# Kernel optimization log

Measured on AMD Instinct MI355X. Metric: run time of the kernel, lower is better.

Reference implementation:

```python
import jax, jax.numpy as jnp
import numpy as np

IN_F = 4096
OUT_F = 4096
SPARSITY = 0.9
NNZ = round((1.0 - SPARSITY) * IN_F * OUT_F)  # 1677722
BATCH = 4096


def setup_inputs() -> dict:
    key = jax.random.key(0)
    k1, k2, k3, k4 = jax.random.split(key, 4)
    x = jax.random.normal(k1, (BATCH, IN_F), dtype=jnp.float32)
    # Kaiming-ish scale for sparse fan-in
    weights = jax.random.normal(k2, (NNZ,), dtype=jnp.float32) * 0.02
    row = jax.random.randint(k3, (NNZ,), 0, OUT_F, dtype=jnp.int32)
    col = jax.random.randint(k4, (NNZ,), 0, IN_F, dtype=jnp.int32)
    indices = jnp.stack([row, col], axis=0)  # (2, nnz) like the torch buffer
    active_mask = jnp.ones((NNZ,), dtype=bool)
    return {
        "x": x,
        "weights": weights,
        "indices": indices,
        "active_mask": active_mask,
        "out_features": OUT_F,
        "in_features": IN_F,
    }


def reference(x, weights, indices, active_mask, out_features, in_features):
    # Torch forward: select active edges, build COO (out,in), coalesce
    # (sums duplicate indices), then y = (W @ x^T)^T.
    # Equivalent math: zero inactive weights, scatter-add into dense W,
    # then a dense matmul. Duplicates are summed by .add, matching coalesce.
    w = jnp.where(active_mask, weights, jnp.zeros((), dtype=weights.dtype))
    W = jnp.zeros((out_features, in_features), dtype=x.dtype)
    W = W.at[indices[0], indices[1]].add(w)  # (out, in)
    return x @ W.T  # (B, out)
```

## Files before the change

kernel.cpp:

```cpp
#include <hip/hip_runtime.h>
#include <cstdint>
#include <cstddef>

#define IN_F  4096
#define OUT_F 4096
#define BATCH 4096

typedef __bf16 bf16_t;
typedef __bf16 bf16x8 __attribute__((ext_vector_type(8)));
typedef float  f32x4  __attribute__((ext_vector_type(4)));

__device__ __forceinline__ unsigned short f32_to_bf16_rne(float f) {
  union { float f; unsigned int u; } v;
  v.f = f;
  unsigned int u = v.u;
  return (unsigned short)((u + 0x7FFFu + ((u >> 16) & 1u)) >> 16);
}

__device__ __forceinline__ uint4 cvt8(float4 a, float4 b) {
  uint4 o;
  o.x = (unsigned)f32_to_bf16_rne(a.x) | ((unsigned)f32_to_bf16_rne(a.y) << 16);
  o.y = (unsigned)f32_to_bf16_rne(a.z) | ((unsigned)f32_to_bf16_rne(a.w) << 16);
  o.z = (unsigned)f32_to_bf16_rne(b.x) | ((unsigned)f32_to_bf16_rne(b.y) << 16);
  o.w = (unsigned)f32_to_bf16_rne(b.z) | ((unsigned)f32_to_bf16_rne(b.w) << 16);
  return o;
}

#define WUNITS ((OUT_F * IN_F) / 8)
#define XUNITS ((BATCH * IN_F) / 8)

__global__ __launch_bounds__(256) void init_zero_cvtx(
    float4* __restrict__ Wf32v, const float4* __restrict__ xin,
    uint4* __restrict__ xbf) {
  const float4 z = {0.f, 0.f, 0.f, 0.f};
  for (int u = blockIdx.x * 256 + threadIdx.x; u < WUNITS + XUNITS;
       u += gridDim.x * 256) {
    if (u < WUNITS) {
      Wf32v[2 * u]     = z;
      Wf32v[2 * u + 1] = z;
    } else {
      const int i = u - WUNITS;
      xbf[i] = cvt8(xin[2 * i], xin[2 * i + 1]);
    }
  }
}

__global__ __launch_bounds__(256) void scatter_kernel(
    const float* __restrict__ w, const int* __restrict__ rows,
    const int* __restrict__ cols, const int* __restrict__ mask,
    float* __restrict__ W, int nnz) {
  int i = blockIdx.x * 256 + threadIdx.x;
  if (i < nnz) {
    if (mask[i] != 0) {
      atomicAdd(&W[(size_t)rows[i] * IN_F + cols[i]], w[i]);
    }
  }
}

__global__ __launch_bounds__(256) void cvt_f32_bf16(
    const float4* __restrict__ in, uint4* __restrict__ out, int n8) {
  int i = blockIdx.x * 256 + threadIdx.x;
  if (i >= n8) return;
  out[i] = cvt8(in[2 * i], in[2 * i + 1]);
}

#define A0_B 0
#define B0_B 32768
#define A1_B 65536
#define B1_B 98304
#define HALF 16384

#define STAGE(Xg, kpos, ldsbase) do {                                          \
  __builtin_amdgcn_global_load_lds(                                            \
    (const __attribute__((address_space(1))) void*)((Xg) + (size_t)srow * 4096 + (kpos) + schunk), \
    (__attribute__((address_space(3))) void*)(lds + (ldsbase) + tid * 16), 16, 0, 0); \
  __builtin_amdgcn_global_load_lds(                                            \
    (const __attribute__((address_space(1))) void*)((Xg) + (size_t)(srow + 128) * 4096 + (kpos) + schunk), \
    (__attribute__((address_space(3))) void*)(lds + (ldsbase) + 8192 + tid * 16), 16, 0, 0); \
} while (0)

#define LDA4(base, mh) do {                                                    \
  a0 = *(const bf16x8*)(lds + (base) + offA[mh][0]);                           \
  a1 = *(const bf16x8*)(lds + (base) + offA[mh][1]);                           \
  a2 = *(const bf16x8*)(lds + (base) + offA[mh][2]);                           \
  a3 = *(const bf16x8*)(lds + (base) + offA[mh][3]);                           \
} while (0)

#define LDB4(base) do {                                                        \
  b0 = *(const bf16x8*)(lds + (base) + offB[0]);                               \
  b1 = *(const bf16x8*)(lds + (base) + offB[1]);                               \
  b2 = *(const bf16x8*)(lds + (base) + offB[2]);                               \
  b3 = *(const bf16x8*)(lds + (base) + offB[3]);                               \
} while (0)

#define MFMA16(mh) do {                                                        \
  acc[(mh)*4+0][0] = __builtin_amdgcn_mfma_f32_16x16x32_bf16(a0, b0, acc[(mh)*4+0][0], 0, 0, 0); \
  acc[(mh)*4+0][1] = __builtin_amdgcn_mfma_f32_16x16x32_bf16(a0, b1, acc[(mh)*4+0][1], 0, 0, 0); \
  acc[(mh)*4+0][2] = __builtin_amdgcn_mfma_f32_16x16x32_bf16(a0, b2, acc[(mh)*4+0][2], 0, 0, 0); \
  acc[(mh)*4+0][3] = __builtin_amdgcn_mfma_f32_16x16x32_bf16(a0, b3, acc[(mh)*4+0][3], 0, 0, 0); \
  acc[(mh)*4+1][0] = __builtin_amdgcn_mfma_f32_16x16x32_bf16(a1, b0, acc[(mh)*4+1][0], 0, 0, 0); \
  acc[(mh)*4+1][1] = __builtin_amdgcn_mfma_f32_16x16x32_bf16(a1, b1, acc[(mh)*4+1][1], 0, 0, 0); \
  acc[(mh)*4+1][2] = __builtin_amdgcn_mfma_f32_16x16x32_bf16(a1, b2, acc[(mh)*4+1][2], 0, 0, 0); \
  acc[(mh)*4+1][3] = __builtin_amdgcn_mfma_f32_16x16x32_bf16(a1, b3, acc[(mh)*4+1][3], 0, 0, 0); \
  acc[(mh)*4+2][0] = __builtin_amdgcn_mfma_f32_16x16x32_bf16(a2, b0, acc[(mh)*4+2][0], 0, 0, 0); \
  acc[(mh)*4+2][1] = __builtin_amdgcn_mfma_f32_16x16x32_bf16(a2, b1, acc[(mh)*4+2][1], 0, 0, 0); \
  acc[(mh)*4+2][2] = __builtin_amdgcn_mfma_f32_16x16x32_bf16(a2, b2, acc[(mh)*4+2][2], 0, 0, 0); \
  acc[(mh)*4+2][3] = __builtin_amdgcn_mfma_f32_16x16x32_bf16(a2, b3, acc[(mh)*4+2][3], 0, 0, 0); \
  acc[(mh)*4+3][0] = __builtin_amdgcn_mfma_f32_16x16x32_bf16(a3, b0, acc[(mh)*4+3][0], 0, 0, 0); \
  acc[(mh)*4+3][1] = __builtin_amdgcn_mfma_f32_16x16x32_bf16(a3, b1, acc[(mh)*4+3][1], 0, 0, 0); \
  acc[(mh)*4+3][2] = __builtin_amdgcn_mfma_f32_16x16x32_bf16(a3, b2, acc[(mh)*4+3][2], 0, 0, 0); \
  acc[(mh)*4+3][3] = __builtin_amdgcn_mfma_f32_16x16x32_bf16(a3, b3, acc[(mh)*4+3][3], 0, 0, 0); \
} while (0)

#define BAR()   __builtin_amdgcn_s_barrier()
#define LGKM0() do { asm volatile("s_waitcnt lgkmcnt(0)" ::: "memory");        \
                     __builtin_amdgcn_sched_barrier(0); } while (0)
#define VM(n)   asm volatile("s_waitcnt vmcnt(" #n ")" ::: "memory")
#define PRIO1() __builtin_amdgcn_s_setprio(1)
#define PRIO0() __builtin_amdgcn_s_setprio(0)

__global__ __launch_bounds__(512, 2) void gemm_bt_8ph(
    const bf16_t* __restrict__ A, const bf16_t* __restrict__ Bm,
    float* __restrict__ C) {
  __shared__ __align__(16) char lds[131072];

  const int tid  = threadIdx.x;
  const int lane = tid & 63;
  const int wave = tid >> 6;
  const int wm   = wave >> 2;
  const int wn   = wave & 3;

  const int sbid = (blockIdx.x & 7) * 32 + (blockIdx.x >> 3);
  const int bm   = sbid >> 4;
  const int bn   = sbid & 15;

  const int frow = lane & 15;
  const int c16  = (lane >> 4) * 16;

  int offA[2][4], offB[4];
#pragma unroll
  for (int mh = 0; mh < 2; ++mh)
#pragma unroll
    for (int mi = 0; mi < 4; ++mi) {
      int r = wm * 128 + mh * 64 + mi * 16 + frow;
      offA[mh][mi] = r * 64 + (c16 ^ (((r >> 1) & 3) << 4));
    }
#pragma unroll
  for (int ni = 0; ni < 4; ++ni) {
    int r = wn * 64 + ni * 16 + frow;
    offB[ni] = r * 64 + (c16 ^ (((r >> 1) & 3) << 4));
  }

  const int srow   = tid >> 2;
  const int schunk = ((tid & 3) ^ ((srow >> 1) & 3)) * 8;
  const bf16_t* Ag = A  + (size_t)bm * 256 * 4096;
  const bf16_t* Bg = Bm + (size_t)bn * 256 * 4096;

  f32x4 acc[8][4] = {};
  bf16x8 a0, a1, a2, a3, b0, b1, b2, b3;

  STAGE(Ag, 0,  A0_B);
  STAGE(Bg, 0,  B0_B);
  STAGE(Ag, 32, A0_B + HALF);
  STAGE(Bg, 32, B0_B + HALF);
  STAGE(Bg, 64, B1_B);
  STAGE(Ag, 64, A1_B);
  STAGE(Bg, 96, B1_B + HALF);
  VM(6);
  BAR();

  int kb = 0;
#pragma unroll 1
  for (int i = 0; i < 31; ++i, kb += 128) {
    LDA4(A0_B, 0); LDB4(B0_B);
    STAGE(Ag, kb + 96, A1_B + HALF);
    BAR(); LGKM0(); PRIO1(); MFMA16(0); PRIO0(); BAR();
    LDA4(A0_B, 1);
    STAGE(Bg, kb + 128, B0_B);
    BAR(); LGKM0(); PRIO1(); MFMA16(1); PRIO0(); VM(10); BAR();
    LDA4(A0_B + HALF, 0); LDB4(B0_B + HALF);
    STAGE(Ag, kb + 128, A0_B);
    BAR(); LGKM0(); PRIO1(); MFMA16(0); PRIO0(); BAR();
    LDA4(A0_B + HALF, 1);
    STAGE(Bg, kb + 160, B0_B + HALF);
    BAR(); LGKM0(); PRIO1(); MFMA16(1); PRIO0(); VM(10); BAR();
    LDA4(A1_B, 0); LDB4(B1_B);
    STAGE(Ag, kb + 160, A0_B + HALF);
    BAR(); LGKM0(); PRIO1(); MFMA16(0); PRIO0(); BAR();
    LDA4(A1_B, 1);
    STAGE(Bg, kb + 192, B1_B);
    BAR(); LGKM0(); PRIO1(); MFMA16(1); PRIO0(); VM(10); BAR();
    LDA4(A1_B + HALF, 0); LDB4(B1_B + HALF);
    STAGE(Ag, kb + 192, A1_B);
    BAR(); LGKM0(); PRIO1(); MFMA16(0); PRIO0(); BAR();
    LDA4(A1_B + HALF, 1);
    STAGE(Bg, kb + 224, B1_B + HALF);
    BAR(); LGKM0(); PRIO1(); MFMA16(1); PRIO0(); VM(10); BAR();
  }

  LDA4(A0_B, 0); LDB4(B0_B);
  STAGE(Ag, 4064, A1_B + HALF);
  BAR(); LGKM0(); PRIO1(); MFMA16(0); PRIO0(); BAR();
  LDA4(A0_B, 1);
  BAR(); LGKM0(); PRIO1(); MFMA16(1); PRIO0(); VM(6); BAR();
  LDA4(A0_B + HALF, 0); LDB4(B0_B + HALF);
  BAR(); LGKM0(); PRIO1(); MFMA16(0); PRIO0(); BAR();
  LDA4(A0_B + HALF, 1);
  BAR(); LGKM0(); PRIO1(); MFMA16(1); PRIO0(); VM(2); BAR();
  LDA4(A1_B, 0); LDB4(B1_B);
  BAR(); LGKM0(); PRIO1(); MFMA16(0); PRIO0(); BAR();
  LDA4(A1_B, 1);
  BAR(); LGKM0(); PRIO1(); MFMA16(1); PRIO0(); VM(0); BAR();
  LDA4(A1_B + HALF, 0); LDB4(B1_B + HALF);
  BAR(); LGKM0(); PRIO1(); MFMA16(0); PRIO0(); BAR();
  LDA4(A1_B + HALF, 1);
  LGKM0(); PRIO1(); MFMA16(1); PRIO0();

#pragma unroll
  for (int mh = 0; mh < 2; ++mh)
#pragma unroll
    for (int mi = 0; mi < 4; ++mi)
#pragma unroll
      for (int ni = 0; ni < 4; ++ni) {
        const int row = bm * 256 + wm * 128 + mh * 64 + mi * 16 + (lane >> 4) * 4;
        const int col = bn * 256 + wn * 64 + ni * 16 + frow;
#pragma unroll
        for (int jj = 0; jj < 4; ++jj)
          C[(size_t)(row + jj) * 4096 + col] = acc[mh * 4 + mi][ni][jj];
      }
}

extern "C" void kernel_launch(void* const* d_in, const int* in_sizes, int n_in,
                              void* d_out, int out_size, void* d_ws, size_t ws_size,
                              hipStream_t stream) {
  const float* x     = (const float*)d_in[0];
  const float* wvals = (const float*)d_in[1];
  const int*   idx   = (const int*)d_in[2];
  const int*   mk    = (const int*)d_in[3];
  const int    nnz   = in_sizes[1];

  float*  Wf32 = (float*)d_out;
  bf16_t* Wbf  = (bf16_t*)d_ws;
  bf16_t* xbf  = (bf16_t*)((char*)d_ws + (size_t)OUT_F * IN_F * sizeof(bf16_t));

  const size_t needed = (size_t)OUT_F * IN_F * 2 + (size_t)BATCH * IN_F * 2;
  if (ws_size < needed) return;

  init_zero_cvtx<<<2048, 256, 0, stream>>>(
      (float4*)Wf32, (const float4*)x, (uint4*)xbf);

  scatter_kernel<<<(nnz + 255) / 256, 256, 0, stream>>>(
      wvals, idx, idx + nnz, mk, Wf32, nnz);

  const int w8 = (OUT_F * IN_F) / 8;
  cvt_f32_bf16<<<(w8 + 255) / 256, 256, 0, stream>>>(
      (const float4*)Wf32, (uint4*)Wbf, w8);

  gemm_bt_8ph<<<256, 512, 0, stream>>>(xbf, Wbf, (float*)d_out);
}
```

Measured before the change: 227.7 us.

## Scatter directly into bf16 weights via packed atomics and merge GEMM phases

The scatter now converts each weight to bf16 and accumulates it directly into a bf16 dense W with global_atomic_pk_add_bf16. This removes the fp32 W zeroing (64 MB of writes) and the separate fp32-to-bf16 conversion pass. Duplicate indices are now summed in bf16, which can change rounding compared with summing in fp32. The GEMM main loop also moves from 8 phases to 4 by loading all A/B fragments at once and issuing 32 MFMAs per phase, with fewer barriers but more registers held live.

```diff
diff --git a/kernel.cpp b/kernel.cpp
--- a/kernel.cpp
+++ b/kernel.cpp
@@ -26,42 +26,37 @@
   return o;
 }
 
-#define WUNITS ((OUT_F * IN_F) / 8)
+#define WU16 ((OUT_F * IN_F) / 8)
 #define XUNITS ((BATCH * IN_F) / 8)
 
 __global__ __launch_bounds__(256) void init_zero_cvtx(
-    float4* __restrict__ Wf32v, const float4* __restrict__ xin,
+    uint4* __restrict__ Wbfv, const float4* __restrict__ xin,
     uint4* __restrict__ xbf) {
-  const float4 z = {0.f, 0.f, 0.f, 0.f};
-  for (int u = blockIdx.x * 256 + threadIdx.x; u < WUNITS + XUNITS;
+  const uint4 z = {0u, 0u, 0u, 0u};
+  for (int u = blockIdx.x * 256 + threadIdx.x; u < WU16 + XUNITS;
        u += gridDim.x * 256) {
-    if (u < WUNITS) {
-      Wf32v[2 * u]     = z;
-      Wf32v[2 * u + 1] = z;
+    if (u < WU16) {
+      Wbfv[u] = z;
     } else {
-      const int i = u - WUNITS;
+      const int i = u - WU16;
       xbf[i] = cvt8(xin[2 * i], xin[2 * i + 1]);
     }
   }
 }
 
-__global__ __launch_bounds__(256) void scatter_kernel(
+__global__ __launch_bounds__(256) void scatter_bf16(
     const float* __restrict__ w, const int* __restrict__ rows,
     const int* __restrict__ cols, const int* __restrict__ mask,
-    float* __restrict__ W, int nnz) {
+    unsigned* __restrict__ Wpk, int nnz) {
   int i = blockIdx.x * 256 + threadIdx.x;
-  if (i < nnz) {
-    if (mask[i] != 0) {
-      atomicAdd(&W[(size_t)rows[i] * IN_F + cols[i]], w[i]);
-    }
-  }
-}
-
-__global__ __launch_bounds__(256) void cvt_f32_bf16(
-    const float4* __restrict__ in, uint4* __restrict__ out, int n8) {
-  int i = blockIdx.x * 256 + threadIdx.x;
-  if (i >= n8) return;
-  out[i] = cvt8(in[2 * i], in[2 * i + 1]);
+  if (i >= nnz) return;
+  if (mask[i] == 0) return;
+  const unsigned h = f32_to_bf16_rne(w[i]);
+  const size_t e = (size_t)rows[i] * IN_F + cols[i];
+  const unsigned data = (e & 1) ? (h << 16) : h;
+  unsigned* p = Wpk + (e >> 1);
+  asm volatile("global_atomic_pk_add_bf16 %0, %1, off"
+               :: "v"(p), "v"(data) : "memory");
 }
 
 #define A0_B 0
@@ -79,38 +74,41 @@
     (__attribute__((address_space(3))) void*)(lds + (ldsbase) + 8192 + tid * 16), 16, 0, 0); \
 } while (0)
 
-#define LDA4(base, mh) do {                                                    \
-  a0 = *(const bf16x8*)(lds + (base) + offA[mh][0]);                           \
-  a1 = *(const bf16x8*)(lds + (base) + offA[mh][1]);                           \
-  a2 = *(const bf16x8*)(lds + (base) + offA[mh][2]);                           \
-  a3 = *(const bf16x8*)(lds + (base) + offA[mh][3]);                           \
+#define LDALL(ab, bb) do {                                                     \
+  a0 = *(const bf16x8*)(lds + (ab) + offA[0][0]);                              \
+  a1 = *(const bf16x8*)(lds + (ab) + offA[0][1]);                              \
+  a2 = *(const bf16x8*)(lds + (ab) + offA[0][2]);                              \
+  a3 = *(const bf16x8*)(lds + (ab) + offA[0][3]);                              \
+  a4 = *(const bf16x8*)(lds + (ab) + offA[1][0]);                              \
+  a5 = *(const bf16x8*)(lds + (ab) + offA[1][1]);                              \
+  a6 = *(const bf16x8*)(lds + (ab) + offA[1][2]);                              \
+  a7 = *(const bf16x8*)(lds + (ab) + offA[1][3]);                              \
+  b0 = *(const bf16x8*)(lds + (bb) + offB[0]);                                 \
+  b1 = *(const bf16x8*)(lds + (bb) + offB[1]);                                 \
+  b2 = *(const bf16x8*)(lds + (bb) + offB[2]);                                 \
+  b3 = *(const bf16x8*)(lds + (bb) + offB[3]);                                 \
 } while (0)
 
-#define LDB4(base) do {                                                        \
-  b0 = *(const bf16x8*)(lds + (base) + offB[0]);                               \
-  b1 = *(const bf16x8*)(lds + (base) + offB[1]);                               \
-  b2 = *(const bf16x8*)(lds + (base) + offB[2]);                               \
-  b3 = *(const bf16x8*)(lds + (base) + offB[3]);                               \
+#define MQ(mh, A0_, A1_, A2_, A3_) do {                                        \
+  acc[(mh)*4+0][0] = __builtin_amdgcn_mfma_f32_16x16x32_bf16(A0_, b0, acc[(mh)*4+0][0], 0, 0, 0); \
+  acc[(mh)*4+0][1] = __builtin_amdgcn_mfma_f32_16x16x32_bf16(A0_, b1, acc[(mh)*4+0][1], 0, 0, 0); \
+  acc[(mh)*4+0][2] = __builtin_amdgcn_mfma_f32_16x16x32_bf16(A0_, b2, acc[(mh)*4+0][2], 0, 0, 0); \
+  acc[(mh)*4+0][3] = __builtin_amdgcn_mfma_f32_16x16x32_bf16(A0_, b3, acc[(mh)*4+0][3], 0, 0, 0); \
+  acc[(mh)*4+1][0] = __builtin_amdgcn_mfma_f32_16x16x32_bf16(A1_, b0, acc[(mh)*4+1][0], 0, 0, 0); \
+  acc[(mh)*4+1][1] = __builtin_amdgcn_mfma_f32_16x16x32_bf16(A1_, b1, acc[(mh)*4+1][1], 0, 0, 0); \
+  acc[(mh)*4+1][2] = __builtin_amdgcn_mfma_f32_16x16x32_bf16(A1_, b2, acc[(mh)*4+1][2], 0, 0, 0); \
+  acc[(mh)*4+1][3] = __builtin_amdgcn_mfma_f32_16x16x32_bf16(A1_, b3, acc[(mh)*4+1][3], 0, 0, 0); \
+  acc[(mh)*4+2][0] = __builtin_amdgcn_mfma_f32_16x16x32_bf16(A2_, b0, acc[(mh)*4+2][0], 0, 0, 0); \
+  acc[(mh)*4+2][1] = __builtin_amdgcn_mfma_f32_16x16x32_bf16(A2_, b1, acc[(mh)*4+2][1], 0, 0, 0); \
+  acc[(mh)*4+2][2] = __builtin_amdgcn_mfma_f32_16x16x32_bf16(A2_, b2, acc[(mh)*4+2][2], 0, 0, 0); \
+  acc[(mh)*4+2][3] = __builtin_amdgcn_mfma_f32_16x16x32_bf16(A2_, b3, acc[(mh)*4+2][3], 0, 0, 0); \
+  acc[(mh)*4+3][0] = __builtin_amdgcn_mfma_f32_16x16x32_bf16(A3_, b0, acc[(mh)*4+3][0], 0, 0, 0); \
+  acc[(mh)*4+3][1] = __builtin_amdgcn_mfma_f32_16x16x32_bf16(A3_, b1, acc[(mh)*4+3][1], 0, 0, 0); \
+  acc[(mh)*4+3][2] = __builtin_amdgcn_mfma_f32_16x16x32_bf16(A3_, b2, acc[(mh)*4+3][2], 0, 0, 0); \
+  acc[(mh)*4+3][3] = __builtin_amdgcn_mfma_f32_16x16x32_bf16(A3_, b3, acc[(mh)*4+3][3], 0, 0, 0); \
 } while (0)
 
-#define MFMA16(mh) do {                                                        \
-  acc[(mh)*4+0][0] = __builtin_amdgcn_mfma_f32_16x16x32_bf16(a0, b0, acc[(mh)*4+0][0], 0, 0, 0); \
-  acc[(mh)*4+0][1] = __builtin_amdgcn_mfma_f32_16x16x32_bf16(a0, b1, acc[(mh)*4+0][1], 0, 0, 0); \
-  acc[(mh)*4+0][2] = __builtin_amdgcn_mfma_f32_16x16x32_bf16(a0, b2, acc[(mh)*4+0][2], 0, 0, 0); \
-  acc[(mh)*4+0][3] = __builtin_amdgcn_mfma_f32_16x16x32_bf16(a0, b3, acc[(mh)*4+0][3], 0, 0, 0); \
-  acc[(mh)*4+1][0] = __builtin_amdgcn_mfma_f32_16x16x32_bf16(a1, b0, acc[(mh)*4+1][0], 0, 0, 0); \
-  acc[(mh)*4+1][1] = __builtin_amdgcn_mfma_f32_16x16x32_bf16(a1, b1, acc[(mh)*4+1][1], 0, 0, 0); \
-  acc[(mh)*4+1][2] = __builtin_amdgcn_mfma_f32_16x16x32_bf16(a1, b2, acc[(mh)*4+1][2], 0, 0, 0); \
-  acc[(mh)*4+1][3] = __builtin_amdgcn_mfma_f32_16x16x32_bf16(a1, b3, acc[(mh)*4+1][3], 0, 0, 0); \
-  acc[(mh)*4+2][0] = __builtin_amdgcn_mfma_f32_16x16x32_bf16(a2, b0, acc[(mh)*4+2][0], 0, 0, 0); \
-  acc[(mh)*4+2][1] = __builtin_amdgcn_mfma_f32_16x16x32_bf16(a2, b1, acc[(mh)*4+2][1], 0, 0, 0); \
-  acc[(mh)*4+2][2] = __builtin_amdgcn_mfma_f32_16x16x32_bf16(a2, b2, acc[(mh)*4+2][2], 0, 0, 0); \
-  acc[(mh)*4+2][3] = __builtin_amdgcn_mfma_f32_16x16x32_bf16(a2, b3, acc[(mh)*4+2][3], 0, 0, 0); \
-  acc[(mh)*4+3][0] = __builtin_amdgcn_mfma_f32_16x16x32_bf16(a3, b0, acc[(mh)*4+3][0], 0, 0, 0); \
-  acc[(mh)*4+3][1] = __builtin_amdgcn_mfma_f32_16x16x32_bf16(a3, b1, acc[(mh)*4+3][1], 0, 0, 0); \
-  acc[(mh)*4+3][2] = __builtin_amdgcn_mfma_f32_16x16x32_bf16(a3, b2, acc[(mh)*4+3][2], 0, 0, 0); \
-  acc[(mh)*4+3][3] = __builtin_amdgcn_mfma_f32_16x16x32_bf16(a3, b3, acc[(mh)*4+3][3], 0, 0, 0); \
-} while (0)
+#define MFMA32() do { MQ(0, a0, a1, a2, a3); MQ(1, a4, a5, a6, a7); } while (0)
 
 #define BAR()   __builtin_amdgcn_s_barrier()
 #define LGKM0() do { asm volatile("s_waitcnt lgkmcnt(0)" ::: "memory");        \
@@ -119,7 +117,7 @@
 #define PRIO1() __builtin_amdgcn_s_setprio(1)
 #define PRIO0() __builtin_amdgcn_s_setprio(0)
 
-__global__ __launch_bounds__(512, 2) void gemm_bt_8ph(
+__global__ __launch_bounds__(512, 2) void gemm_bt_4ph(
     const bf16_t* __restrict__ A, const bf16_t* __restrict__ Bm,
     float* __restrict__ C) {
   __shared__ __align__(16) char lds[131072];
@@ -157,64 +155,48 @@
   const bf16_t* Bg = Bm + (size_t)bn * 256 * 4096;
 
   f32x4 acc[8][4] = {};
-  bf16x8 a0, a1, a2, a3, b0, b1, b2, b3;
+  bf16x8 a0, a1, a2, a3, a4, a5, a6, a7, b0, b1, b2, b3;
 
   STAGE(Ag, 0,  A0_B);
   STAGE(Bg, 0,  B0_B);
   STAGE(Ag, 32, A0_B + HALF);
   STAGE(Bg, 32, B0_B + HALF);
+  STAGE(Ag, 64, A1_B);
   STAGE(Bg, 64, B1_B);
-  STAGE(Ag, 64, A1_B);
-  STAGE(Bg, 96, B1_B + HALF);
-  VM(6);
+  VM(8);
   BAR();
 
   int kb = 0;
 #pragma unroll 1
   for (int i = 0; i < 31; ++i, kb += 128) {
-    LDA4(A0_B, 0); LDB4(B0_B);
+    LDALL(A0_B, B0_B);
     STAGE(Ag, kb + 96, A1_B + HALF);
-    BAR(); LGKM0(); PRIO1(); MFMA16(0); PRIO0(); BAR();
-    LDA4(A0_B, 1);
+    STAGE(Bg, kb + 96, B1_B + HALF);
+    BAR(); LGKM0(); PRIO1(); MFMA32(); PRIO0(); VM(8); BAR();
+    LDALL(A0_B + HALF, B0_B + HALF);
+    STAGE(Ag, kb + 128, A0_B);
     STAGE(Bg, kb + 128, B0_B);
-    BAR(); LGKM0(); PRIO1(); MFMA16(1); PRIO0(); VM(10); BAR();
-    LDA4(A0_B + HALF, 0); LDB4(B0_B + HALF);
-    STAGE(Ag, kb + 128, A0_B);
-    BAR(); LGKM0(); PRIO1(); MFMA16(0); PRIO0(); BAR();
-    LDA4(A0_B + HALF, 1);
+    BAR(); LGKM0(); PRIO1(); MFMA32(); PRIO0(); VM(8); BAR();
+    LDALL(A1_B, B1_B);
+    STAGE(Ag, kb + 160, A0_B + HALF);
     STAGE(Bg, kb + 160, B0_B + HALF);
-    BAR(); LGKM0(); PRIO1(); MFMA16(1); PRIO0(); VM(10); BAR();
-    LDA4(A1_B, 0); LDB4(B1_B);
-    STAGE(Ag, kb + 160, A0_B + HALF);
-    BAR(); LGKM0(); PRIO1(); MFMA16(0); PRIO0(); BAR();
-    LDA4(A1_B, 1);
+    BAR(); LGKM0(); PRIO1(); MFMA32(); PRIO0(); VM(8); BAR();
+    LDALL(A1_B + HALF, B1_B + HALF);
+    STAGE(Ag, kb + 192, A1_B);
     STAGE(Bg, kb + 192, B1_B);
-    BAR(); LGKM0(); PRIO1(); MFMA16(1); PRIO0(); VM(10); BAR();
-    LDA4(A1_B + HALF, 0); LDB4(B1_B + HALF);
-    STAGE(Ag, kb + 192, A1_B);
-    BAR(); LGKM0(); PRIO1(); MFMA16(0); PRIO0(); BAR();
-    LDA4(A1_B + HALF, 1);
-    STAGE(Bg, kb + 224, B1_B + HALF);
-    BAR(); LGKM0(); PRIO1(); MFMA16(1); PRIO0(); VM(10); BAR();
+    BAR(); LGKM0(); PRIO1(); MFMA32(); PRIO0(); VM(8); BAR();
   }
 
-  LDA4(A0_B, 0); LDB4(B0_B);
+  LDALL(A0_B, B0_B);
   STAGE(Ag, 4064, A1_B + HALF);
-  BAR(); LGKM0(); PRIO1(); MFMA16(0); PRIO0(); BAR();
-  LDA4(A0_B, 1);
-  BAR(); LGKM0(); PRIO1(); MFMA16(1); PRIO0(); VM(6); BAR();
-  LDA4(A0_B + HALF, 0); LDB4(B0_B + HALF);
-  BAR(); LGKM0(); PRIO1(); MFMA16(0); PRIO0(); BAR();
-  LDA4(A0_B + HALF, 1);
-  BAR(); LGKM0(); PRIO1(); MFMA16(1); PRIO0(); VM(2); BAR();
-  LDA4(A1_B, 0); LDB4(B1_B);
-  BAR(); LGKM0(); PRIO1(); MFMA16(0); PRIO0(); BAR();
-  LDA4(A1_B, 1);
-  BAR(); LGKM0(); PRIO1(); MFMA16(1); PRIO0(); VM(0); BAR();
-  LDA4(A1_B + HALF, 0); LDB4(B1_B + HALF);
-  BAR(); LGKM0(); PRIO1(); MFMA16(0); PRIO0(); BAR();
-  LDA4(A1_B + HALF, 1);
-  LGKM0(); PRIO1(); MFMA16(1); PRIO0();
+  STAGE(Bg, 4064, B1_B + HALF);
+  BAR(); LGKM0(); PRIO1(); MFMA32(); PRIO0(); VM(8); BAR();
+  LDALL(A0_B + HALF, B0_B + HALF);
+  BAR(); LGKM0(); PRIO1(); MFMA32(); PRIO0(); VM(4); BAR();
+  LDALL(A1_B, B1_B);
+  BAR(); LGKM0(); PRIO1(); MFMA32(); PRIO0(); VM(0); BAR();
+  LDALL(A1_B + HALF, B1_B + HALF);
+  LGKM0(); PRIO1(); MFMA32(); PRIO0();
 
 #pragma unroll
   for (int mh = 0; mh < 2; ++mh)
@@ -239,22 +221,17 @@
   const int*   mk    = (const int*)d_in[3];
   const int    nnz   = in_sizes[1];
 
-  float*  Wf32 = (float*)d_out;
-  bf16_t* Wbf  = (bf16_t*)d_ws;
-  bf16_t* xbf  = (bf16_t*)((char*)d_ws + (size_t)OUT_F * IN_F * sizeof(bf16_t));
+  bf16_t* Wbf = (bf16_t*)d_ws;
+  bf16_t* xbf = (bf16_t*)((char*)d_ws + (size_t)OUT_F * IN_F * sizeof(bf16_t));
 
   const size_t needed = (size_t)OUT_F * IN_F * 2 + (size_t)BATCH * IN_F * 2;
   if (ws_size < needed) return;
 
   init_zero_cvtx<<<2048, 256, 0, stream>>>(
-      (float4*)Wf32, (const float4*)x, (uint4*)xbf);
-
-  scatter_kernel<<<(nnz + 255) / 256, 256, 0, stream>>>(
-      wvals, idx, idx + nnz, mk, Wf32, nnz);
-
-  const int w8 = (OUT_F * IN_F) / 8;
-  cvt_f32_bf16<<<(w8 + 255) / 256, 256, 0, stream>>>(
-      (const float4*)Wf32, (uint4*)Wbf, w8);
-
-  gemm_bt_8ph<<<256, 512, 0, stream>>>(xbf, Wbf, (float*)d_out);
-}
+      (uint4*)Wbf, (const float4*)x, (uint4*)xbf);
+
+  scatter_bf16<<<(nnz + 255) / 256, 256, 0, stream>>>(
+      wvals, idx, idx + nnz, mk, (unsigned*)Wbf, nnz);
+
+  gemm_bt_4ph<<<256, 512, 0, stream>>>(xbf, Wbf, (float*)d_out);
+}
```

After: 212.3 us. 6.8% less time.
